# Optimization experiments

Hardware: AMD Instinct MI355X
Metric: run time of the kernel (lower is better)

The kernel has to match this reference:

```python
import jax, jax.numpy as jnp
import numpy as np

GAMMA = 0.5

def setup_inputs() -> dict:
    key = jax.random.key(0)
    k1, k2 = jax.random.split(key)
    x = jax.random.normal(k1, (4096, 256), dtype=jnp.float32)
    W = jax.random.normal(k2, (256, 512), dtype=jnp.float32)
    return {"x": x, "W": W}

def reference(x, W):
    # difference: (B, D, N) = (B, D, 1) - (D, N)
    diff = x[:, :, None] - W[None, :, :]
    sq_dist = jnp.sum(diff * diff, axis=1)          # (B, N)
    return jnp.exp(-GAMMA * sq_dist)                # (B, N)
```

## Files before the change

### kernel.cpp

```cpp
#include <hip/hip_runtime.h>


#define GAMMA 0.5f
#define B_  4096
#define D_  256
#define N_  512
#define BM  64
#define BN  32
#define LDT 264

typedef __attribute__((ext_vector_type(8))) short bf16x8;
typedef __attribute__((ext_vector_type(4))) float f32x4;
typedef __attribute__((ext_vector_type(4))) unsigned short u16x4;
typedef __attribute__((ext_vector_type(4))) float float4v;

__device__ __forceinline__ unsigned short f2bf(float f) {
    union { float f; unsigned int i; } u; u.f = f;
    return (unsigned short)(u.i >> 16);
}
__device__ __forceinline__ float bf2f(unsigned short h) {
    union { unsigned int i; float f; } u; u.i = ((unsigned int)h) << 16;
    return u.f;
}

__global__ __launch_bounds__(256, 2)
void rbf_kernel(const float* __restrict__ x, const float* __restrict__ W,
                float* __restrict__ out) {
    __shared__ unsigned short xs[BM][LDT];
    __shared__ unsigned short ws[BN][LDT];
    __shared__ float x2s[BM];
    __shared__ float w2s[BN];

    const int tid = threadIdx.x;
    const int bx = blockIdx.x;
    const int by = blockIdx.y;

    {
        const float4v* xg = (const float4v*)(x + (size_t)by * BM * D_);
        for (int i = tid; i < BM * (D_ / 4); i += 256) {
            int r = i >> 6, c4 = i & 63;
            float4v v = xg[i];
            u16x4 p = { f2bf(v.x), f2bf(v.y), f2bf(v.z), f2bf(v.w) };
            *(u16x4*)&xs[r][c4 * 4] = p;
        }
    }

    {
        const float* Wg = W + bx * BN;
        for (int i = tid; i < (D_ / 4) * (BN / 4); i += 256) {
            int kb = i >> 3, nb = i & 7;
            const float* p0 = Wg + (size_t)(kb * 4) * N_ + nb * 4;
            float4v r0 = *(const float4v*)(p0);
            float4v r1 = *(const float4v*)(p0 + N_);
            float4v r2 = *(const float4v*)(p0 + 2 * N_);
            float4v r3 = *(const float4v*)(p0 + 3 * N_);
            u16x4 c0 = { f2bf(r0.x), f2bf(r1.x), f2bf(r2.x), f2bf(r3.x) };
            u16x4 c1 = { f2bf(r0.y), f2bf(r1.y), f2bf(r2.y), f2bf(r3.y) };
            u16x4 c2 = { f2bf(r0.z), f2bf(r1.z), f2bf(r2.z), f2bf(r3.z) };
            u16x4 c3 = { f2bf(r0.w), f2bf(r1.w), f2bf(r2.w), f2bf(r3.w) };
            *(u16x4*)&ws[nb * 4 + 0][kb * 4] = c0;
            *(u16x4*)&ws[nb * 4 + 1][kb * 4] = c1;
            *(u16x4*)&ws[nb * 4 + 2][kb * 4] = c2;
            *(u16x4*)&ws[nb * 4 + 3][kb * 4] = c3;
        }
    }
    __syncthreads();

    {
        int row = tid >> 2, q = tid & 3;
        float s = 0.f;
        for (int c = 0; c < 8; ++c) {
            bf16x8 v = *(const bf16x8*)&xs[row][q * 64 + c * 8];
            #pragma unroll
            for (int j = 0; j < 8; ++j) { float f = bf2f((unsigned short)v[j]); s += f * f; }
        }
        s += __shfl_xor(s, 1);
        s += __shfl_xor(s, 2);
        if (q == 0) x2s[row] = s;

        if (tid < BN * 4) {
            int col = tid >> 2;
            float t2 = 0.f;
            for (int c = 0; c < 8; ++c) {
                bf16x8 v = *(const bf16x8*)&ws[col][q * 64 + c * 8];
                #pragma unroll
                for (int j = 0; j < 8; ++j) { float f = bf2f((unsigned short)v[j]); t2 += f * f; }
            }
            t2 += __shfl_xor(t2, 1);
            t2 += __shfl_xor(t2, 2);
            if (q == 0) w2s[col] = t2;
        }
    }
    __syncthreads();

    const int l = tid & 63, w = tid >> 6;
    const int wr = w >> 1, wc = w & 1;
    const int lr = l & 15, g = l >> 4;

    f32x4 acc00 = {0.f, 0.f, 0.f, 0.f};
    f32x4 acc10 = {0.f, 0.f, 0.f, 0.f};
    #pragma unroll
    for (int kk = 0; kk < 8; ++kk) {
        int ko = kk * 32 + g * 8;
        bf16x8 a0 = *(const bf16x8*)&xs[wr * 32 + lr][ko];
        bf16x8 a1 = *(const bf16x8*)&xs[wr * 32 + 16 + lr][ko];
        bf16x8 b0 = *(const bf16x8*)&ws[wc * 16 + lr][ko];
        acc00 = __builtin_amdgcn_mfma_f32_16x16x32_bf16(a0, b0, acc00, 0, 0, 0);
        acc10 = __builtin_amdgcn_mfma_f32_16x16x32_bf16(a1, b0, acc10, 0, 0, 0);
    }

    const float c2l = -(GAMMA) * 1.4426950408889634f;
    float* outp = out + (size_t)(by * BM) * N_ + bx * BN;
    #pragma unroll
    for (int m = 0; m < 2; ++m) {
        f32x4 a = m ? acc10 : acc00;
        #pragma unroll
        for (int i = 0; i < 4; ++i) {
            int ar = wr * 32 + m * 16 + g * 4 + i;
            int ac = wc * 16 + lr;
            float s = x2s[ar] + w2s[ac] - 2.f * a[i];
            outp[(size_t)ar * N_ + ac] = exp2f(s * c2l);
        }
    }
}

extern "C" void kernel_launch(void* const* d_in, const int* in_sizes, int n_in,
                              void* d_out, int out_size, void* d_ws, size_t ws_size,
                              hipStream_t stream) {
    const float* x = (const float*)d_in[0];
    const float* W = (const float*)d_in[1];
    float* out = (float*)d_out;
    dim3 grid(N_ / BN, B_ / BM);
    rbf_kernel<<<grid, dim3(256), 0, stream>>>(x, W, out);
}
```

Baseline: 72.57 us.

## Load W directly into MFMA registers, widen N tile, swizzle block order

Removes the shared-memory staging and transpose of W: each lane reads its W column fragment straight from global memory, converts it to bf16 in registers, and computes the squared column norm (in fp32, from the unrounded values) with wave shuffles. The N tile grows to 64 so each wave runs a 2x2 set of MFMAs, the grid is flattened to 512 blocks with a swizzled block-to-tile mapping, and the launch bound now asks for occupancy 4. This cuts LDS traffic and one load phase, but the strided per-element global W loads could be poorly coalesced and may raise latency.

```diff
diff --git a/kernel.cpp b/kernel.cpp
--- a/kernel.cpp
+++ b/kernel.cpp
@@ -6,7 +6,7 @@
 #define D_  256
 #define N_  512
 #define BM  64
-#define BN  32
+#define BN  64
 #define LDT 264
 
 typedef __attribute__((ext_vector_type(8))) short bf16x8;
@@ -23,45 +23,28 @@
     return u.f;
 }
 
-__global__ __launch_bounds__(256, 2)
+__global__ __launch_bounds__(256, 4)
 void rbf_kernel(const float* __restrict__ x, const float* __restrict__ W,
                 float* __restrict__ out) {
     __shared__ unsigned short xs[BM][LDT];
-    __shared__ unsigned short ws[BN][LDT];
     __shared__ float x2s[BM];
-    __shared__ float w2s[BN];
 
     const int tid = threadIdx.x;
-    const int bx = blockIdx.x;
-    const int by = blockIdx.y;
+
+    const int bid = blockIdx.x;
+    const int wgid = (bid & 7) * 64 + (bid >> 3);
+    const int bx = wgid & 7;
+    const int by = wgid >> 3;
 
     {
         const float4v* xg = (const float4v*)(x + (size_t)by * BM * D_);
-        for (int i = tid; i < BM * (D_ / 4); i += 256) {
+        #pragma unroll
+        for (int t = 0; t < 16; ++t) {
+            int i = tid + t * 256;
             int r = i >> 6, c4 = i & 63;
             float4v v = xg[i];
             u16x4 p = { f2bf(v.x), f2bf(v.y), f2bf(v.z), f2bf(v.w) };
             *(u16x4*)&xs[r][c4 * 4] = p;
-        }
-    }
-
-    {
-        const float* Wg = W + bx * BN;
-        for (int i = tid; i < (D_ / 4) * (BN / 4); i += 256) {
-            int kb = i >> 3, nb = i & 7;
-            const float* p0 = Wg + (size_t)(kb * 4) * N_ + nb * 4;
-            float4v r0 = *(const float4v*)(p0);
-            float4v r1 = *(const float4v*)(p0 + N_);
-            float4v r2 = *(const float4v*)(p0 + 2 * N_);
-            float4v r3 = *(const float4v*)(p0 + 3 * N_);
-            u16x4 c0 = { f2bf(r0.x), f2bf(r1.x), f2bf(r2.x), f2bf(r3.x) };
-            u16x4 c1 = { f2bf(r0.y), f2bf(r1.y), f2bf(r2.y), f2bf(r3.y) };
-            u16x4 c2 = { f2bf(r0.z), f2bf(r1.z), f2bf(r2.z), f2bf(r3.z) };
-            u16x4 c3 = { f2bf(r0.w), f2bf(r1.w), f2bf(r2.w), f2bf(r3.w) };
-            *(u16x4*)&ws[nb * 4 + 0][kb * 4] = c0;
-            *(u16x4*)&ws[nb * 4 + 1][kb * 4] = c1;
-            *(u16x4*)&ws[nb * 4 + 2][kb * 4] = c2;
-            *(u16x4*)&ws[nb * 4 + 3][kb * 4] = c3;
         }
     }
     __syncthreads();
@@ -69,6 +52,7 @@
     {
         int row = tid >> 2, q = tid & 3;
         float s = 0.f;
+        #pragma unroll
         for (int c = 0; c < 8; ++c) {
             bf16x8 v = *(const bf16x8*)&xs[row][q * 64 + c * 8];
             #pragma unroll
@@ -77,19 +61,6 @@
         s += __shfl_xor(s, 1);
         s += __shfl_xor(s, 2);
         if (q == 0) x2s[row] = s;
-
-        if (tid < BN * 4) {
-            int col = tid >> 2;
-            float t2 = 0.f;
-            for (int c = 0; c < 8; ++c) {
-                bf16x8 v = *(const bf16x8*)&ws[col][q * 64 + c * 8];
-                #pragma unroll
-                for (int j = 0; j < 8; ++j) { float f = bf2f((unsigned short)v[j]); t2 += f * f; }
-            }
-            t2 += __shfl_xor(t2, 1);
-            t2 += __shfl_xor(t2, 2);
-            if (q == 0) w2s[col] = t2;
-        }
     }
     __syncthreads();
 
@@ -97,29 +68,51 @@
     const int wr = w >> 1, wc = w & 1;
     const int lr = l & 15, g = l >> 4;
 
-    f32x4 acc00 = {0.f, 0.f, 0.f, 0.f};
-    f32x4 acc10 = {0.f, 0.f, 0.f, 0.f};
+    const float* Wg = W + bx * BN + wc * 32 + lr;
+    float w2p0 = 0.f, w2p1 = 0.f;
+    f32x4 accs[2][2] = {{{0,0,0,0},{0,0,0,0}},{{0,0,0,0},{0,0,0,0}}};
+
     #pragma unroll
     for (int kk = 0; kk < 8; ++kk) {
-        int ko = kk * 32 + g * 8;
-        bf16x8 a0 = *(const bf16x8*)&xs[wr * 32 + lr][ko];
-        bf16x8 a1 = *(const bf16x8*)&xs[wr * 32 + 16 + lr][ko];
-        bf16x8 b0 = *(const bf16x8*)&ws[wc * 16 + lr][ko];
-        acc00 = __builtin_amdgcn_mfma_f32_16x16x32_bf16(a0, b0, acc00, 0, 0, 0);
-        acc10 = __builtin_amdgcn_mfma_f32_16x16x32_bf16(a1, b0, acc10, 0, 0, 0);
+        const int k0 = kk * 32 + g * 8;
+        const float* wp = Wg + (size_t)k0 * N_;
+        float w0[8], w1[8];
+        #pragma unroll
+        for (int j = 0; j < 8; ++j) {
+            w0[j] = wp[(size_t)j * N_];
+            w1[j] = wp[(size_t)j * N_ + 16];
+        }
+        bf16x8 b0, b1;
+        #pragma unroll
+        for (int j = 0; j < 8; ++j) {
+            b0[j] = (short)f2bf(w0[j]); b1[j] = (short)f2bf(w1[j]);
+            w2p0 += w0[j] * w0[j];      w2p1 += w1[j] * w1[j];
+        }
+        bf16x8 a0 = *(const bf16x8*)&xs[wr * 32 + lr][k0];
+        bf16x8 a1 = *(const bf16x8*)&xs[wr * 32 + 16 + lr][k0];
+        accs[0][0] = __builtin_amdgcn_mfma_f32_16x16x32_bf16(a0, b0, accs[0][0], 0, 0, 0);
+        accs[0][1] = __builtin_amdgcn_mfma_f32_16x16x32_bf16(a0, b1, accs[0][1], 0, 0, 0);
+        accs[1][0] = __builtin_amdgcn_mfma_f32_16x16x32_bf16(a1, b0, accs[1][0], 0, 0, 0);
+        accs[1][1] = __builtin_amdgcn_mfma_f32_16x16x32_bf16(a1, b1, accs[1][1], 0, 0, 0);
     }
+
+    w2p0 += __shfl_xor(w2p0, 16); w2p0 += __shfl_xor(w2p0, 32);
+    w2p1 += __shfl_xor(w2p1, 16); w2p1 += __shfl_xor(w2p1, 32);
 
     const float c2l = -(GAMMA) * 1.4426950408889634f;
     float* outp = out + (size_t)(by * BM) * N_ + bx * BN;
     #pragma unroll
     for (int m = 0; m < 2; ++m) {
-        f32x4 a = m ? acc10 : acc00;
         #pragma unroll
-        for (int i = 0; i < 4; ++i) {
-            int ar = wr * 32 + m * 16 + g * 4 + i;
-            int ac = wc * 16 + lr;
-            float s = x2s[ar] + w2s[ac] - 2.f * a[i];
-            outp[(size_t)ar * N_ + ac] = exp2f(s * c2l);
+        for (int n = 0; n < 2; ++n) {
+            float w2v = n ? w2p1 : w2p0;
+            int ac = wc * 32 + n * 16 + lr;
+            #pragma unroll
+            for (int i = 0; i < 4; ++i) {
+                int ar = wr * 32 + m * 16 + g * 4 + i;
+                float s = x2s[ar] + w2v - 2.f * accs[m][n][i];
+                outp[(size_t)ar * N_ + ac] = exp2f(s * c2l);
+            }
         }
     }
 }
@@ -130,6 +123,5 @@
     const float* x = (const float*)d_in[0];
     const float* W = (const float*)d_in[1];
     float* out = (float*)d_out;
-    dim3 grid(N_ / BN, B_ / BM);
-    rbf_kernel<<<grid, dim3(256), 0, stream>>>(x, W, out);
+    rbf_kernel<<<dim3(512), dim3(256), 0, stream>>>(x, W, out);
 }
```

After: 61.79 us. 1.17x faster.
